# Kernel optimization log

Hardware: AMD Instinct MI355X
Metric: run time of the kernel (lower is better)

Reference implementation:

```python
import jax, jax.numpy as jnp
import numpy as np
import math

D = 2048
N1 = 250  # fixed by fc1 = Linear(250, 1)
N2 = 27   # fixed by fc2 = Linear(27, 1) for img_size=96


def setup_inputs() -> dict:
    key = jax.random.key(0)
    ks = jax.random.split(key, 18)
    s = 0.02
    def w(k, shape):
        return jax.random.normal(k, shape, dtype=jnp.float32) * s
    return {
        "input_tensor1": jax.random.normal(ks[0], (N1, D), dtype=jnp.float32),
        "input_tensor2": jax.random.normal(ks[1], (N2, D), dtype=jnp.float32),
        "Wq1": w(ks[2], (D, D)), "bq1": jnp.zeros((D,), jnp.float32),
        "Wk1": w(ks[3], (D, D)), "bk1": jnp.zeros((D,), jnp.float32),
        "Wv1": w(ks[4], (D, D)), "bv1": jnp.zeros((D,), jnp.float32),
        "Wq2": w(ks[5], (D, D)), "bq2": jnp.zeros((D,), jnp.float32),
        "Wk2": w(ks[6], (D, D)), "bk2": jnp.zeros((D,), jnp.float32),
        "Wv2": w(ks[7], (D, D)), "bv2": jnp.zeros((D,), jnp.float32),
        "w_fc1": w(ks[8], (N1,)), "b_fc1": jnp.zeros((), jnp.float32),
        "w_fc2": w(ks[9], (N2,)), "b_fc2": jnp.zeros((), jnp.float32),
    }


def reference(input_tensor1, input_tensor2,
              Wq1, bq1, Wk1, bk1, Wv1, bv1,
              Wq2, bq2, Wk2, bk2, Wv2, bv2,
              w_fc1, b_fc1, w_fc2, b_fc2):
    d = input_tensor1.shape[1]
    q1 = input_tensor1 @ Wq1.T + bq1  # [N1, D]
    k1 = input_tensor1 @ Wk1.T + bk1
    v1 = input_tensor1 @ Wv1.T + bv1
    q2 = input_tensor2 @ Wq2.T + bq2  # [N2, D]
    k2 = input_tensor2 @ Wk2.T + bk2
    v2 = input_tensor2 @ Wv2.T + bv2
    scale = 1.0 / math.sqrt(d)

    # sigmoid cross-attention scores
    probs1 = jax.nn.sigmoid((q2 @ k1.T) * scale)  # [N2, N1]
    probs2 = jax.nn.sigmoid((q1 @ k2.T) * scale)  # [N1, N2]

    # Original builds whole[t, i, d] = probs1[t, i] * v2[t, d] then applies
    # fc1 (Linear(N1,1)) along i: ctx1[t,d] = v2[t,d] * (probs1[t,:] @ w_fc1) + b_fc1.
    # Fused form avoids the [N2, N1, D] intermediate; math identical.
    context_layer1 = v2 * (probs1 @ w_fc1)[:, None] + b_fc1  # [N2, D]
    context_layer2 = v1 * (probs2 @ w_fc2)[:, None] + b_fc2  # [N1, D]

    return (context_layer2, probs2, context_layer1, probs1)
```

## Files before the change

### kernel.cpp

```cpp
#include <hip/hip_runtime.h>

typedef unsigned short u16;
typedef unsigned int u32;
typedef __attribute__((ext_vector_type(8))) short short8;
typedef __attribute__((ext_vector_type(4))) float f32x4;

#define DD 2048
constexpr int OFF_P2   = 512000;
constexpr int OFF_CTX1 = 518750;
constexpr int OFF_P1   = 574046;

__device__ __forceinline__ u16 f2bf(float f){
  u32 u = __float_as_uint(f);
  u += 0x7fffu + ((u >> 16) & 1u);
  return (u16)(u >> 16);
}
__device__ __forceinline__ float bf2f(u32 us){
  return __uint_as_float(us << 16);
}
__device__ __forceinline__ u32 pk(float a, float b){
  return (u32)f2bf(a) | ((u32)f2bf(b) << 16);
}

__global__ __launch_bounds__(256) void k_gemm_nt(
    const float* __restrict__ in1, const float* __restrict__ in2,
    const float* __restrict__ Wv1, const float* __restrict__ bv1,
    const float* __restrict__ Wq2, const float* __restrict__ bq2,
    const float* __restrict__ Wk2, const float* __restrict__ bk2,
    const float* __restrict__ Wv2, const float* __restrict__ bv2,
    float* __restrict__ outv1, u16* __restrict__ q2b, u16* __restrict__ k2b,
    float* __restrict__ v2f)
{
  __shared__ u16 lds_a[64*72];
  __shared__ u16 lds_b[64*72];
  const int b = blockIdx.x, t = threadIdx.x;
  const float *A, *B, *bias;
  int Mreal, m0, n0, kind;
  if (b < 128){
    A = in1; Mreal = 250; m0 = (b>>5)*64; n0 = (b&31)*64; B = Wv1; bias = bv1; kind = 0;
  } else {
    int s = b - 128, mat = s>>5;
    n0 = (s&31)*64; A = in2; Mreal = 27; m0 = 0;
    B    = (mat==0) ? Wq2 : ((mat==1) ? Wk2 : Wv2);
    bias = (mat==0) ? bq2 : ((mat==1) ? bk2 : bv2);
    kind = 1 + mat;
  }
  const int w = t>>6, l = t&63, wm = w>>1, wn = w&1;
  const int srow = t>>4, scol = (t&15)*4;
  float4 pfa[4], pfb[4];

  auto loadt = [&](int k0){
#pragma unroll
    for (int p=0;p<4;p++){
      int row = p*16 + srow;
      int gm = m0 + row;
      if (gm < Mreal) pfa[p] = *(const float4*)&A[(size_t)gm*DD + k0 + scol];
      else { pfa[p].x=0.f; pfa[p].y=0.f; pfa[p].z=0.f; pfa[p].w=0.f; }
      pfb[p] = *(const float4*)&B[(size_t)(n0+row)*DD + k0 + scol];
    }
  };

  f32x4 acc[2][2];
#pragma unroll
  for (int i=0;i<2;i++)
#pragma unroll
    for (int j=0;j<2;j++) acc[i][j] = (f32x4){0.f,0.f,0.f,0.f};

  loadt(0);
#pragma unroll 1
  for (int kt=0; kt<32; ++kt){
    __syncthreads();
#pragma unroll
    for (int p=0;p<4;p++){
      int row = p*16 + srow;
      uint2 av; av.x = pk(pfa[p].x, pfa[p].y); av.y = pk(pfa[p].z, pfa[p].w);
      *(uint2*)&lds_a[row*72 + scol] = av;
      uint2 bw; bw.x = pk(pfb[p].x, pfb[p].y); bw.y = pk(pfb[p].z, pfb[p].w);
      *(uint2*)&lds_b[row*72 + scol] = bw;
    }
    __syncthreads();
    if (kt < 31) loadt((kt+1)*64);
#pragma unroll
    for (int kk=0; kk<2; ++kk){
      const int kf = kk*32 + (l>>4)*8;
      short8 af[2], bfr[2];
#pragma unroll
      for (int mf=0;mf<2;mf++) af[mf]  = *(const short8*)&lds_a[(wm*32+mf*16+(l&15))*72 + kf];
#pragma unroll
      for (int nf=0;nf<2;nf++) bfr[nf] = *(const short8*)&lds_b[(wn*32+nf*16+(l&15))*72 + kf];
#pragma unroll
      for (int mf=0;mf<2;mf++)
#pragma unroll
        for (int nf=0;nf<2;nf++)
          acc[mf][nf] = __builtin_amdgcn_mfma_f32_16x16x32_bf16(af[mf], bfr[nf], acc[mf][nf], 0, 0, 0);
    }
  }
#pragma unroll
  for (int mf=0;mf<2;mf++)
#pragma unroll
    for (int nf=0;nf<2;nf++){
      int colg = n0 + wn*32 + nf*16 + (l&15);
      float bv = bias[colg];
#pragma unroll
      for (int r=0;r<4;r++){
        int m = m0 + wm*32 + mf*16 + ((l>>4)<<2) + r;
        if (m < Mreal){
          float v = acc[mf][nf][r] + bv;
          size_t off = (size_t)m*DD + colg;
          if (kind == 0)      outv1[off] = v;
          else if (kind == 1) q2b[off] = f2bf(v);
          else if (kind == 2) k2b[off] = f2bf(v);
          else                v2f[off] = v;
        }
      }
    }
}

__global__ __launch_bounds__(256) void k_gemm_nn(
    const u16* __restrict__ q2b, const u16* __restrict__ k2b,
    const float* __restrict__ Wk1, const float* __restrict__ Wq1,
    float* __restrict__ t1f, float* __restrict__ t2f)
{
  __shared__ u16 lds_a[32*72];
  __shared__ u16 lds_b[64*36];
  const int b = blockIdx.x, t = threadIdx.x;
  const int mat = b>>7, rem = b&127, nt = rem>>1, ks = rem&1;
  const int n0 = nt*32, kbase = ks*1024;
  const u16* A = mat ? k2b : q2b;
  const float* B = mat ? Wq1 : Wk1;
  float* OUT = mat ? t2f : t1f;
  const int w = t>>6, l = t&63, mf = w>>1, nf = w&1;
  const int arow = t>>3, acol8 = (t&7)*8;
  uint4 pa; float4 pb[2];
  auto loadt = [&](int k0){
    if (arow < 27) pa = *(const uint4*)&A[(size_t)arow*DD + k0 + acol8];
    else { pa.x=0u; pa.y=0u; pa.z=0u; pa.w=0u; }
#pragma unroll
    for (int p=0;p<2;p++){
      int idx = p*256 + t, rk = idx>>3, c4 = (idx&7)*4;
      pb[p] = *(const float4*)&B[(size_t)(k0+rk)*DD + n0 + c4];
    }
  };
  f32x4 acc = (f32x4){0.f,0.f,0.f,0.f};
  loadt(kbase);
#pragma unroll 1
  for (int kt=0; kt<16; ++kt){
    __syncthreads();
    *(uint4*)&lds_a[arow*72 + acol8] = pa;
#pragma unroll
    for (int p=0;p<2;p++){
      int idx = p*256 + t, rk = idx>>3, c4 = (idx&7)*4;
      uint2 bv; bv.x = pk(pb[p].x, pb[p].y); bv.y = pk(pb[p].z, pb[p].w);
      *(uint2*)&lds_b[rk*36 + c4] = bv;
    }
    __syncthreads();
    if (kt < 15) loadt(kbase + (kt+1)*64);
#pragma unroll
    for (int kk=0; kk<2; ++kk){
      const int kf = kk*32 + (l>>4)*8;
      short8 af = *(const short8*)&lds_a[(mf*16+(l&15))*72 + kf];
      short8 bfr;
      const int n = nf*16 + (l&15);
#pragma unroll
      for (int j=0;j<8;j++) bfr[j] = (short)lds_b[(kf+j)*36 + n];
      acc = __builtin_amdgcn_mfma_f32_16x16x32_bf16(af, bfr, acc, 0, 0, 0);
    }
  }
  const int col = n0 + nf*16 + (l&15);
#pragma unroll
  for (int r=0;r<4;r++){
    int row = mf*16 + ((l>>4)<<2) + r;
    atomicAdd(&OUT[(size_t)row*DD + col], acc[r]);
  }
}

__global__ __launch_bounds__(256) void k_sgemm(
    const float* __restrict__ t1f, const float* __restrict__ t2f,
    const float* __restrict__ in1,
    const u16* __restrict__ q2b, const u16* __restrict__ k2b,
    const float* __restrict__ bk1, const float* __restrict__ bq1,
    float* __restrict__ S1f, float* __restrict__ S2f,
    float* __restrict__ c1acc, float* __restrict__ r2acc)
{
  __shared__ u16 lds_a[32*72];
  __shared__ u16 lds_b[64*72];
  const int b = blockIdx.x, t = threadIdx.x;
  const int w = t>>6, l = t&63;
  if (b < 256){
    const int mat = b>>7, rem = b&127, jt = rem>>5, ks = rem&31;
    const int j0 = jt*64, kbase = ks*64;
    const float* Af = mat ? t2f : t1f;
    float* OUT = mat ? S2f : S1f;
#pragma unroll
    for (int p=0;p<2;p++){
      int f4i = p*256 + t, row = f4i>>4, c4 = (f4i&15)*4;
      float4 v = *(const float4*)&Af[(size_t)row*DD + kbase + c4];
      uint2 pv; pv.x = pk(v.x, v.y); pv.y = pk(v.z, v.w);
      *(uint2*)&lds_a[row*72 + c4] = pv;
    }
#pragma unroll
    for (int p=0;p<4;p++){
      int f4i = p*256 + t, row = f4i>>4, c4 = (f4i&15)*4;
      int j = j0 + row;
      float4 v;
      if (j < 250) v = *(const float4*)&in1[(size_t)j*DD + kbase + c4];
      else { v.x=0.f; v.y=0.f; v.z=0.f; v.w=0.f; }
      uint2 pv; pv.x = pk(v.x, v.y); pv.y = pk(v.z, v.w);
      *(uint2*)&lds_b[row*72 + c4] = pv;
    }
    __syncthreads();
    const int wm = w>>1, wn = w&1;
    f32x4 acc[2];
    acc[0] = (f32x4){0.f,0.f,0.f,0.f};
    acc[1] = (f32x4){0.f,0.f,0.f,0.f};
#pragma unroll
    for (int kk=0; kk<2; ++kk){
      const int kf = kk*32 + (l>>4)*8;
      short8 af = *(const short8*)&lds_a[(wm*16+(l&15))*72 + kf];
#pragma unroll
      for (int nf=0;nf<2;nf++){
        short8 bfr = *(const short8*)&lds_b[(wn*32+nf*16+(l&15))*72 + kf];
        acc[nf] = __builtin_amdgcn_mfma_f32_16x16x32_bf16(af, bfr, acc[nf], 0, 0, 0);
      }
    }
#pragma unroll
    for (int nf=0;nf<2;nf++){
      int col = j0 + wn*32 + nf*16 + (l&15);
#pragma unroll
      for (int r=0;r<4;r++){
        int row = wm*16 + ((l>>4)<<2) + r;
        atomicAdd(&OUT[row*256 + col], acc[nf][r]);
      }
    }
  } else {
    const int s = b - 256, mat = s>>3, kc = s&7, kbase = kc*256;
    const u16* Ab = mat ? k2b : q2b;
    const float* bias = mat ? bq1 : bk1;
    float* OUT = mat ? r2acc : c1acc;
    for (int tt = w; tt < 27; tt += 4){
      int e = kbase + l*4;
      uint2 aa = *(const uint2*)&Ab[(size_t)tt*DD + e];
      float4 bb = *(const float4*)&bias[e];
      float sum = bf2f(aa.x & 0xffffu)*bb.x + bf2f(aa.x >> 16)*bb.y
                + bf2f(aa.y & 0xffffu)*bb.z + bf2f(aa.y >> 16)*bb.w;
#pragma unroll
      for (int off=32; off; off>>=1) sum += __shfl_xor(sum, off);
      if (l == 0) atomicAdd(&OUT[tt], sum);
    }
  }
}

__global__ __launch_bounds__(256) void k_finish(
    const float* __restrict__ S1f, const float* __restrict__ S2f,
    const float* __restrict__ c1acc, const float* __restrict__ r2acc,
    const float* __restrict__ w_fc1, const float* __restrict__ w_fc2,
    const float* __restrict__ b_fc1p, const float* __restrict__ b_fc2p,
    float* __restrict__ g1acc, float* __restrict__ d_out)
{
  const int b = blockIdx.x, t = threadIdx.x, w = t>>6, l = t&63;
  const int j = b*4 + w;
  if (j >= 250) return;
  const float scale = 0.022097086912079608f;
  if (l < 27){
    float s1 = (S1f[l*256 + j] + c1acc[l]) * scale;
    float p1 = 1.f / (1.f + expf(-s1));
    d_out[OFF_P1 + l*250 + j] = p1;
    atomicAdd(&g1acc[l], p1 * w_fc1[j]);
  }
  float gv = 0.f;
  if (l < 27){
    float s2 = (S2f[l*256 + j] + r2acc[l]) * scale;
    float p2 = 1.f / (1.f + expf(-s2));
    d_out[OFF_P2 + j*27 + l] = p2;
    gv = p2 * w_fc2[l];
  }
#pragma unroll
  for (int off=32; off; off>>=1) gv += __shfl_xor(gv, off);
  const float g2 = gv, bfc2 = b_fc2p[0];
#pragma unroll
  for (int i=0;i<8;i++){
    int e4 = l + 64*i;
    float4 v = *(const float4*)&d_out[(size_t)j*DD + e4*4];
    v.x = v.x*g2 + bfc2; v.y = v.y*g2 + bfc2;
    v.z = v.z*g2 + bfc2; v.w = v.w*g2 + bfc2;
    *(float4*)&d_out[(size_t)j*DD + e4*4] = v;
  }
}

__global__ __launch_bounds__(256) void k_ctx1(
    const float* __restrict__ g1acc, const float* __restrict__ b_fc1p,
    float* __restrict__ d_out)
{
  const int i = blockIdx.x*256 + threadIdx.x;
  if (i >= 27*1024) return;
  const int row = i >> 10, c2 = (i & 1023)*2;
  const float g = g1acc[row], bb = b_fc1p[0];
  float* p = &d_out[OFF_CTX1 + (size_t)row*DD + c2];
  float2 v = *(const float2*)p;
  v.x = v.x*g + bb; v.y = v.y*g + bb;
  *(float2*)p = v;
}

extern "C" void kernel_launch(void* const* d_in, const int* in_sizes, int n_in,
                              void* d_out, int out_size, void* d_ws, size_t ws_size,
                              hipStream_t stream)
{
  const float* in1 = (const float*)d_in[0];
  const float* in2 = (const float*)d_in[1];
  const float* Wq1 = (const float*)d_in[2];  const float* bq1 = (const float*)d_in[3];
  const float* Wk1 = (const float*)d_in[4];  const float* bk1 = (const float*)d_in[5];
  const float* Wv1 = (const float*)d_in[6];  const float* bv1 = (const float*)d_in[7];
  const float* Wq2 = (const float*)d_in[8];  const float* bq2 = (const float*)d_in[9];
  const float* Wk2 = (const float*)d_in[10]; const float* bk2 = (const float*)d_in[11];
  const float* Wv2 = (const float*)d_in[12]; const float* bv2 = (const float*)d_in[13];
  const float* wfc1 = (const float*)d_in[14]; const float* bfc1 = (const float*)d_in[15];
  const float* wfc2 = (const float*)d_in[16]; const float* bfc2 = (const float*)d_in[17];
  float* out = (float*)d_out;

  float* ws    = (float*)d_ws;
  float* g1acc = ws;
  float* c1acc = ws + 32;
  float* r2acc = ws + 64;
  float* S1f   = ws + 96;
  float* S2f   = S1f + 32*256;
  float* t1f   = S2f + 32*256;
  float* t2f   = t1f + 32*2048;
  float* zend  = t2f + 32*2048;
  u16*   q2b   = (u16*)zend;
  u16*   k2b   = q2b + 32*2048;
  float* v2f   = out + OFF_CTX1;

  hipMemsetAsync(d_ws, 0, (size_t)((char*)zend - (char*)d_ws), stream);
  k_gemm_nt<<<224, 256, 0, stream>>>(in1, in2, Wv1, bv1, Wq2, bq2, Wk2, bk2,
                                     Wv2, bv2, out, q2b, k2b, v2f);
  k_gemm_nn<<<256, 256, 0, stream>>>(q2b, k2b, Wk1, Wq1, t1f, t2f);
  k_sgemm<<<272, 256, 0, stream>>>(t1f, t2f, in1, q2b, k2b, bk1, bq1,
                                   S1f, S2f, c1acc, r2acc);
  k_finish<<<63, 256, 0, stream>>>(S1f, S2f, c1acc, r2acc, wfc1, wfc2,
                                   bfc1, bfc2, g1acc, out);
  k_ctx1<<<108, 256, 0, stream>>>(g1acc, bfc1, out);
}
```

Before: 206.5 us.

## Compute all six projections directly with split-K partials, drop associativity chain

Replaces the q2·Wk1 reassociation chain with direct computation of q1, k1 and v1 alongside q2, k2 and v2 in one batched split-K GEMM kernel. Partial sums are written to separate workspace slices and reduced by consumers, which removes atomics and most of the memset. The score kernel sums the partials on load and writes split-K score partials that the finish kernel reduces. This adds FLOPs for the 250-row projections and extra partial-buffer traffic in exchange for fewer dependent stages and more parallelism.

```diff
diff --git a/kernel.cpp b/kernel.cpp
--- a/kernel.cpp
+++ b/kernel.cpp
@@ -10,41 +10,52 @@
 constexpr int OFF_CTX1 = 518750;
 constexpr int OFF_P1   = 574046;
 
+constexpr int SLB = 512000;
+constexpr int SLS = 55296;
+constexpr int Q1P = 0;
+constexpr int K1P = 1024000;
+constexpr int V1P = 2048000;
+constexpr int Q2P = 3072000;
+constexpr int K2P = Q2P + 4*SLS;
+constexpr int V2P = K2P + 4*SLS;
+constexpr int S1P = V2P + 4*SLS;
+constexpr int S2P = S1P + 8*8192;
+constexpr int G1A = S2P + 8*8192;
+
 __device__ __forceinline__ u16 f2bf(float f){
   u32 u = __float_as_uint(f);
   u += 0x7fffu + ((u >> 16) & 1u);
   return (u16)(u >> 16);
 }
-__device__ __forceinline__ float bf2f(u32 us){
-  return __uint_as_float(us << 16);
-}
 __device__ __forceinline__ u32 pk(float a, float b){
   return (u32)f2bf(a) | ((u32)f2bf(b) << 16);
 }
 
-__global__ __launch_bounds__(256) void k_gemm_nt(
+struct P6 { const float* W[6]; const float* b[6]; };
+
+__global__ __launch_bounds__(256) void k6nt(
     const float* __restrict__ in1, const float* __restrict__ in2,
-    const float* __restrict__ Wv1, const float* __restrict__ bv1,
-    const float* __restrict__ Wq2, const float* __restrict__ bq2,
-    const float* __restrict__ Wk2, const float* __restrict__ bk2,
-    const float* __restrict__ Wv2, const float* __restrict__ bv2,
-    float* __restrict__ outv1, u16* __restrict__ q2b, u16* __restrict__ k2b,
-    float* __restrict__ v2f)
+    P6 par, float* __restrict__ ws)
 {
   __shared__ u16 lds_a[64*72];
   __shared__ u16 lds_b[64*72];
   const int b = blockIdx.x, t = threadIdx.x;
-  const float *A, *B, *bias;
-  int Mreal, m0, n0, kind;
-  if (b < 128){
-    A = in1; Mreal = 250; m0 = (b>>5)*64; n0 = (b&31)*64; B = Wv1; bias = bv1; kind = 0;
+  const float* A; int Mreal, m0, n0, kbase, KT, g; float* outp;
+  if (b < 768){
+    g = b >> 8; int r = b & 255;
+    m0 = (r >> 6) * 64; int r2 = r & 63; n0 = (r2 >> 1) * 64; int ks = r2 & 1;
+    A = in1; Mreal = 250; kbase = ks * 1024; KT = 16;
+    outp = ws + g * (2*SLB) + ks * SLB;
   } else {
-    int s = b - 128, mat = s>>5;
-    n0 = (s&31)*64; A = in2; Mreal = 27; m0 = 0;
-    B    = (mat==0) ? Wq2 : ((mat==1) ? Wk2 : Wv2);
-    bias = (mat==0) ? bq2 : ((mat==1) ? bk2 : bv2);
-    kind = 1 + mat;
-  }
+    int s = b - 768; g = 3 + s / 128; int r = s % 128;
+    n0 = (r >> 2) * 64; int ks = r & 3;
+    A = in2; Mreal = 27; m0 = 0; kbase = ks * 512; KT = 8;
+    outp = ws + Q2P + (g - 3) * (4*SLS) + ks * SLS;
+  }
+  const bool addb = (kbase == 0);
+  const float* Bw = par.W[g];
+  const float* bias = par.b[g];
+
   const int w = t>>6, l = t&63, wm = w>>1, wn = w&1;
   const int srow = t>>4, scol = (t&15)*4;
   float4 pfa[4], pfb[4];
@@ -56,7 +67,7 @@
       int gm = m0 + row;
       if (gm < Mreal) pfa[p] = *(const float4*)&A[(size_t)gm*DD + k0 + scol];
       else { pfa[p].x=0.f; pfa[p].y=0.f; pfa[p].z=0.f; pfa[p].w=0.f; }
-      pfb[p] = *(const float4*)&B[(size_t)(n0+row)*DD + k0 + scol];
+      pfb[p] = *(const float4*)&Bw[(size_t)(n0+row)*DD + k0 + scol];
     }
   };
 
@@ -66,9 +77,9 @@
 #pragma unroll
     for (int j=0;j<2;j++) acc[i][j] = (f32x4){0.f,0.f,0.f,0.f};
 
-  loadt(0);
+  loadt(kbase);
 #pragma unroll 1
-  for (int kt=0; kt<32; ++kt){
+  for (int kt=0; kt<KT; ++kt){
     __syncthreads();
 #pragma unroll
     for (int p=0;p<4;p++){
@@ -79,7 +90,7 @@
       *(uint2*)&lds_b[row*72 + scol] = bw;
     }
     __syncthreads();
-    if (kt < 31) loadt((kt+1)*64);
+    if (kt < KT-1) loadt(kbase + (kt+1)*64);
 #pragma unroll
     for (int kk=0; kk<2; ++kk){
       const int kf = kk*32 + (l>>4)*8;
@@ -100,101 +111,46 @@
 #pragma unroll
     for (int nf=0;nf<2;nf++){
       int colg = n0 + wn*32 + nf*16 + (l&15);
-      float bv = bias[colg];
+      float bv = addb ? bias[colg] : 0.f;
 #pragma unroll
       for (int r=0;r<4;r++){
         int m = m0 + wm*32 + mf*16 + ((l>>4)<<2) + r;
-        if (m < Mreal){
-          float v = acc[mf][nf][r] + bv;
-          size_t off = (size_t)m*DD + colg;
-          if (kind == 0)      outv1[off] = v;
-          else if (kind == 1) q2b[off] = f2bf(v);
-          else if (kind == 2) k2b[off] = f2bf(v);
-          else                v2f[off] = v;
-        }
-      }
-    }
-}
-
-__global__ __launch_bounds__(256) void k_gemm_nn(
-    const u16* __restrict__ q2b, const u16* __restrict__ k2b,
-    const float* __restrict__ Wk1, const float* __restrict__ Wq1,
-    float* __restrict__ t1f, float* __restrict__ t2f)
-{
-  __shared__ u16 lds_a[32*72];
-  __shared__ u16 lds_b[64*36];
-  const int b = blockIdx.x, t = threadIdx.x;
-  const int mat = b>>7, rem = b&127, nt = rem>>1, ks = rem&1;
-  const int n0 = nt*32, kbase = ks*1024;
-  const u16* A = mat ? k2b : q2b;
-  const float* B = mat ? Wq1 : Wk1;
-  float* OUT = mat ? t2f : t1f;
-  const int w = t>>6, l = t&63, mf = w>>1, nf = w&1;
-  const int arow = t>>3, acol8 = (t&7)*8;
-  uint4 pa; float4 pb[2];
-  auto loadt = [&](int k0){
-    if (arow < 27) pa = *(const uint4*)&A[(size_t)arow*DD + k0 + acol8];
-    else { pa.x=0u; pa.y=0u; pa.z=0u; pa.w=0u; }
-#pragma unroll
-    for (int p=0;p<2;p++){
-      int idx = p*256 + t, rk = idx>>3, c4 = (idx&7)*4;
-      pb[p] = *(const float4*)&B[(size_t)(k0+rk)*DD + n0 + c4];
-    }
-  };
-  f32x4 acc = (f32x4){0.f,0.f,0.f,0.f};
-  loadt(kbase);
-#pragma unroll 1
-  for (int kt=0; kt<16; ++kt){
-    __syncthreads();
-    *(uint4*)&lds_a[arow*72 + acol8] = pa;
-#pragma unroll
-    for (int p=0;p<2;p++){
-      int idx = p*256 + t, rk = idx>>3, c4 = (idx&7)*4;
-      uint2 bv; bv.x = pk(pb[p].x, pb[p].y); bv.y = pk(pb[p].z, pb[p].w);
-      *(uint2*)&lds_b[rk*36 + c4] = bv;
-    }
-    __syncthreads();
-    if (kt < 15) loadt(kbase + (kt+1)*64);
-#pragma unroll
-    for (int kk=0; kk<2; ++kk){
-      const int kf = kk*32 + (l>>4)*8;
-      short8 af = *(const short8*)&lds_a[(mf*16+(l&15))*72 + kf];
-      short8 bfr;
-      const int n = nf*16 + (l&15);
-#pragma unroll
-      for (int j=0;j<8;j++) bfr[j] = (short)lds_b[(kf+j)*36 + n];
-      acc = __builtin_amdgcn_mfma_f32_16x16x32_bf16(af, bfr, acc, 0, 0, 0);
-    }
-  }
-  const int col = n0 + nf*16 + (l&15);
-#pragma unroll
-  for (int r=0;r<4;r++){
-    int row = mf*16 + ((l>>4)<<2) + r;
-    atomicAdd(&OUT[(size_t)row*DD + col], acc[r]);
-  }
-}
-
-__global__ __launch_bounds__(256) void k_sgemm(
-    const float* __restrict__ t1f, const float* __restrict__ t2f,
-    const float* __restrict__ in1,
-    const u16* __restrict__ q2b, const u16* __restrict__ k2b,
-    const float* __restrict__ bk1, const float* __restrict__ bq1,
-    float* __restrict__ S1f, float* __restrict__ S2f,
-    float* __restrict__ c1acc, float* __restrict__ r2acc)
+        if (m < Mreal) outp[(size_t)m*DD + colg] = acc[mf][nf][r] + bv;
+      }
+    }
+}
+
+__global__ __launch_bounds__(256) void kS(float* __restrict__ ws)
 {
   __shared__ u16 lds_a[32*72];
   __shared__ u16 lds_b[64*72];
   const int b = blockIdx.x, t = threadIdx.x;
-  const int w = t>>6, l = t&63;
-  if (b < 256){
-    const int mat = b>>7, rem = b&127, jt = rem>>5, ks = rem&31;
-    const int j0 = jt*64, kbase = ks*64;
-    const float* Af = mat ? t2f : t1f;
-    float* OUT = mat ? S2f : S1f;
+  const int mat = b>>5, r = b&31, jt = r>>3, ks = r&7;
+  const int j0 = jt*64, kbase = ks*256;
+  const float* Ap = ws + (mat ? K2P : Q2P);
+  const float* Bp = ws + (mat ? Q1P : K1P);
+  float* OUT = ws + (mat ? S2P : S1P) + ks*8192;
+  const int w = t>>6, l = t&63, wm = w>>1, wn = w&1;
+  f32x4 acc[2];
+  acc[0] = (f32x4){0.f,0.f,0.f,0.f};
+  acc[1] = (f32x4){0.f,0.f,0.f,0.f};
+#pragma unroll 1
+  for (int kt=0; kt<4; ++kt){
+    const int kc = kbase + kt*64;
+    __syncthreads();
 #pragma unroll
     for (int p=0;p<2;p++){
       int f4i = p*256 + t, row = f4i>>4, c4 = (f4i&15)*4;
-      float4 v = *(const float4*)&Af[(size_t)row*DD + kbase + c4];
+      float4 v; v.x=0.f; v.y=0.f; v.z=0.f; v.w=0.f;
+      if (row < 27){
+        const float* base = Ap + (size_t)row*DD + kc + c4;
+        float4 v0 = *(const float4*)(base);
+        float4 v1 = *(const float4*)(base + SLS);
+        float4 v2 = *(const float4*)(base + 2*SLS);
+        float4 v3 = *(const float4*)(base + 3*SLS);
+        v.x = (v0.x+v1.x)+(v2.x+v3.x); v.y = (v0.y+v1.y)+(v2.y+v3.y);
+        v.z = (v0.z+v1.z)+(v2.z+v3.z); v.w = (v0.w+v1.w)+(v2.w+v3.w);
+      }
       uint2 pv; pv.x = pk(v.x, v.y); pv.y = pk(v.z, v.w);
       *(uint2*)&lds_a[row*72 + c4] = pv;
     }
@@ -202,17 +158,17 @@
     for (int p=0;p<4;p++){
       int f4i = p*256 + t, row = f4i>>4, c4 = (f4i&15)*4;
       int j = j0 + row;
-      float4 v;
-      if (j < 250) v = *(const float4*)&in1[(size_t)j*DD + kbase + c4];
-      else { v.x=0.f; v.y=0.f; v.z=0.f; v.w=0.f; }
+      float4 v; v.x=0.f; v.y=0.f; v.z=0.f; v.w=0.f;
+      if (j < 250){
+        const float* base = Bp + (size_t)j*DD + kc + c4;
+        float4 v0 = *(const float4*)(base);
+        float4 v1 = *(const float4*)(base + SLB);
+        v.x = v0.x+v1.x; v.y = v0.y+v1.y; v.z = v0.z+v1.z; v.w = v0.w+v1.w;
+      }
       uint2 pv; pv.x = pk(v.x, v.y); pv.y = pk(v.z, v.w);
       *(uint2*)&lds_b[row*72 + c4] = pv;
     }
     __syncthreads();
-    const int wm = w>>1, wn = w&1;
-    f32x4 acc[2];
-    acc[0] = (f32x4){0.f,0.f,0.f,0.f};
-    acc[1] = (f32x4){0.f,0.f,0.f,0.f};
 #pragma unroll
     for (int kk=0; kk<2; ++kk){
       const int kf = kk*32 + (l>>4)*8;
@@ -223,36 +179,20 @@
         acc[nf] = __builtin_amdgcn_mfma_f32_16x16x32_bf16(af, bfr, acc[nf], 0, 0, 0);
       }
     }
-#pragma unroll
-    for (int nf=0;nf<2;nf++){
-      int col = j0 + wn*32 + nf*16 + (l&15);
-#pragma unroll
-      for (int r=0;r<4;r++){
-        int row = wm*16 + ((l>>4)<<2) + r;
-        atomicAdd(&OUT[row*256 + col], acc[nf][r]);
-      }
-    }
-  } else {
-    const int s = b - 256, mat = s>>3, kc = s&7, kbase = kc*256;
-    const u16* Ab = mat ? k2b : q2b;
-    const float* bias = mat ? bq1 : bk1;
-    float* OUT = mat ? r2acc : c1acc;
-    for (int tt = w; tt < 27; tt += 4){
-      int e = kbase + l*4;
-      uint2 aa = *(const uint2*)&Ab[(size_t)tt*DD + e];
-      float4 bb = *(const float4*)&bias[e];
-      float sum = bf2f(aa.x & 0xffffu)*bb.x + bf2f(aa.x >> 16)*bb.y
-                + bf2f(aa.y & 0xffffu)*bb.z + bf2f(aa.y >> 16)*bb.w;
-#pragma unroll
-      for (int off=32; off; off>>=1) sum += __shfl_xor(sum, off);
-      if (l == 0) atomicAdd(&OUT[tt], sum);
+  }
+#pragma unroll
+  for (int nf=0;nf<2;nf++){
+    int col = j0 + wn*32 + nf*16 + (l&15);
+#pragma unroll
+    for (int rr=0;rr<4;rr++){
+      int row = wm*16 + ((l>>4)<<2) + rr;
+      OUT[row*256 + col] = acc[nf][rr];
     }
   }
 }
 
 __global__ __launch_bounds__(256) void k_finish(
-    const float* __restrict__ S1f, const float* __restrict__ S2f,
-    const float* __restrict__ c1acc, const float* __restrict__ r2acc,
+    const float* __restrict__ ws,
     const float* __restrict__ w_fc1, const float* __restrict__ w_fc2,
     const float* __restrict__ b_fc1p, const float* __restrict__ b_fc2p,
     float* __restrict__ g1acc, float* __restrict__ d_out)
@@ -261,44 +201,60 @@
   const int j = b*4 + w;
   if (j >= 250) return;
   const float scale = 0.022097086912079608f;
-  if (l < 27){
-    float s1 = (S1f[l*256 + j] + c1acc[l]) * scale;
-    float p1 = 1.f / (1.f + expf(-s1));
-    d_out[OFF_P1 + l*250 + j] = p1;
-    atomicAdd(&g1acc[l], p1 * w_fc1[j]);
-  }
   float gv = 0.f;
   if (l < 27){
-    float s2 = (S2f[l*256 + j] + r2acc[l]) * scale;
-    float p2 = 1.f / (1.f + expf(-s2));
+    const float* S1p = ws + S1P;
+    const float* S2p = ws + S2P;
+    float s1 = 0.f, s2 = 0.f;
+#pragma unroll
+    for (int p=0;p<8;p++){
+      s1 += S1p[p*8192 + l*256 + j];
+      s2 += S2p[p*8192 + l*256 + j];
+    }
+    float p1 = 1.f / (1.f + expf(-s1*scale));
+    float p2 = 1.f / (1.f + expf(-s2*scale));
+    d_out[OFF_P1 + l*250 + j] = p1;
     d_out[OFF_P2 + j*27 + l] = p2;
+    atomicAdd(&g1acc[l], p1 * w_fc1[j]);
     gv = p2 * w_fc2[l];
   }
 #pragma unroll
   for (int off=32; off; off>>=1) gv += __shfl_xor(gv, off);
   const float g2 = gv, bfc2 = b_fc2p[0];
+  const float* v1a = ws + V1P;
+  const float* v1b = ws + V1P + SLB;
 #pragma unroll
   for (int i=0;i<8;i++){
-    int e4 = l + 64*i;
-    float4 v = *(const float4*)&d_out[(size_t)j*DD + e4*4];
-    v.x = v.x*g2 + bfc2; v.y = v.y*g2 + bfc2;
-    v.z = v.z*g2 + bfc2; v.w = v.w*g2 + bfc2;
-    *(float4*)&d_out[(size_t)j*DD + e4*4] = v;
+    int e4 = (l + 64*i)*4;
+    float4 va = *(const float4*)&v1a[(size_t)j*DD + e4];
+    float4 vb = *(const float4*)&v1b[(size_t)j*DD + e4];
+    float4 o;
+    o.x = (va.x+vb.x)*g2 + bfc2; o.y = (va.y+vb.y)*g2 + bfc2;
+    o.z = (va.z+vb.z)*g2 + bfc2; o.w = (va.w+vb.w)*g2 + bfc2;
+    *(float4*)&d_out[(size_t)j*DD + e4] = o;
   }
 }
 
 __global__ __launch_bounds__(256) void k_ctx1(
-    const float* __restrict__ g1acc, const float* __restrict__ b_fc1p,
-    float* __restrict__ d_out)
+    const float* __restrict__ ws, const float* __restrict__ g1acc,
+    const float* __restrict__ b_fc1p, float* __restrict__ d_out)
 {
   const int i = blockIdx.x*256 + threadIdx.x;
-  if (i >= 27*1024) return;
-  const int row = i >> 10, c2 = (i & 1023)*2;
+  if (i >= 27*512) return;
+  const int row = i >> 9, c4 = (i & 511)*4;
+  const float* v2p = ws + V2P;
+  const float* base = v2p + (size_t)row*DD + c4;
+  float4 v0 = *(const float4*)(base);
+  float4 v1 = *(const float4*)(base + SLS);
+  float4 v2 = *(const float4*)(base + 2*SLS);
+  float4 v3 = *(const float4*)(base + 3*SLS);
   const float g = g1acc[row], bb = b_fc1p[0];
-  float* p = &d_out[OFF_CTX1 + (size_t)row*DD + c2];
-  float2 v = *(const float2*)p;
-  v.x = v.x*g + bb; v.y = v.y*g + bb;
-  *(float2*)p = v;
+  float4 o;
+  o.x = ((v0.x+v1.x)+(v2.x+v3.x))*g + bb;
+  o.y = ((v0.y+v1.y)+(v2.y+v3.y))*g + bb;
+  o.z = ((v0.z+v1.z)+(v2.z+v3.z))*g + bb;
+  o.w = ((v0.w+v1.w)+(v2.w+v3.w))*g + bb;
+  *(float4*)&d_out[OFF_CTX1 + (size_t)row*DD + c4] = o;
 }
 
 extern "C" void kernel_launch(void* const* d_in, const int* in_sizes, int n_in,
@@ -307,36 +263,22 @@
 {
   const float* in1 = (const float*)d_in[0];
   const float* in2 = (const float*)d_in[1];
-  const float* Wq1 = (const float*)d_in[2];  const float* bq1 = (const float*)d_in[3];
-  const float* Wk1 = (const float*)d_in[4];  const float* bk1 = (const float*)d_in[5];
-  const float* Wv1 = (const float*)d_in[6];  const float* bv1 = (const float*)d_in[7];
-  const float* Wq2 = (const float*)d_in[8];  const float* bq2 = (const float*)d_in[9];
-  const float* Wk2 = (const float*)d_in[10]; const float* bk2 = (const float*)d_in[11];
-  const float* Wv2 = (const float*)d_in[12]; const float* bv2 = (const float*)d_in[13];
+  P6 par;
+  par.W[0] = (const float*)d_in[2];  par.b[0] = (const float*)d_in[3];
+  par.W[1] = (const float*)d_in[4];  par.b[1] = (const float*)d_in[5];
+  par.W[2] = (const float*)d_in[6];  par.b[2] = (const float*)d_in[7];
+  par.W[3] = (const float*)d_in[8];  par.b[3] = (const float*)d_in[9];
+  par.W[4] = (const float*)d_in[10]; par.b[4] = (const float*)d_in[11];
+  par.W[5] = (const float*)d_in[12]; par.b[5] = (const float*)d_in[13];
   const float* wfc1 = (const float*)d_in[14]; const float* bfc1 = (const float*)d_in[15];
   const float* wfc2 = (const float*)d_in[16]; const float* bfc2 = (const float*)d_in[17];
   float* out = (float*)d_out;
-
-  float* ws    = (float*)d_ws;
-  float* g1acc = ws;
-  float* c1acc = ws + 32;
-  float* r2acc = ws + 64;
-  float* S1f   = ws + 96;
-  float* S2f   = S1f + 32*256;
-  float* t1f   = S2f + 32*256;
-  float* t2f   = t1f + 32*2048;
-  float* zend  = t2f + 32*2048;
-  u16*   q2b   = (u16*)zend;
-  u16*   k2b   = q2b + 32*2048;
-  float* v2f   = out + OFF_CTX1;
-
-  hipMemsetAsync(d_ws, 0, (size_t)((char*)zend - (char*)d_ws), stream);
-  k_gemm_nt<<<224, 256, 0, stream>>>(in1, in2, Wv1, bv1, Wq2, bq2, Wk2, bk2,
-                                     Wv2, bv2, out, q2b, k2b, v2f);
-  k_gemm_nn<<<256, 256, 0, stream>>>(q2b, k2b, Wk1, Wq1, t1f, t2f);
-  k_sgemm<<<272, 256, 0, stream>>>(t1f, t2f, in1, q2b, k2b, bk1, bq1,
-                                   S1f, S2f, c1acc, r2acc);
-  k_finish<<<63, 256, 0, stream>>>(S1f, S2f, c1acc, r2acc, wfc1, wfc2,
-                                   bfc1, bfc2, g1acc, out);
-  k_ctx1<<<108, 256, 0, stream>>>(g1acc, bfc1, out);
-}
+  float* ws  = (float*)d_ws;
+  float* g1acc = ws + G1A;
+
+  hipMemsetAsync(g1acc, 0, 32*sizeof(float), stream);
+  k6nt<<<1152, 256, 0, stream>>>(in1, in2, par, ws);
+  kS<<<64, 256, 0, stream>>>(ws);
+  k_finish<<<63, 256, 0, stream>>>(ws, wfc1, wfc2, bfc1, bfc2, g1acc, out);
+  k_ctx1<<<54, 256, 0, stream>>>(ws, g1acc, bfc1, out);
+}
```

After: 205.8 us. About the same (-0.3%).
